# Kernel optimization log

Measured on AMD Instinct MI355X. Metric: run time of the kernel, lower is better.

The kernel has to match this reference:

```python
import jax, jax.numpy as jnp
import numpy as np
import math

NUM_SYN = 1000
NUM_MEM = 100
TAU_MIN, TAU_MAX = 10.0, 1000.0
TAU_S = 5.0
DELTA_T = 1.0
LAMBDA = 3.0

def _kappas():
    kappa_s = np.float32(np.exp(-DELTA_T / TAU_S))  # scalar (tau_s uniform)
    tau_m = np.logspace(math.log10(TAU_MIN + 1e-06), math.log10(TAU_MAX - 1e-06), NUM_MEM)
    kappa_m = np.exp(-DELTA_T / np.clip(tau_m, 1e-06, None)).astype(np.float32)
    return kappa_s, jnp.asarray(kappa_m)

def custom_tanh(x):
    return jnp.tanh(x * (2.0 / 3.0)) * 1.7159

def setup_inputs() -> dict:
    key = jax.random.key(0)
    ks = jax.random.split(key, 5)
    B, T = 128, 1024
    H = 2 * NUM_MEM  # 200
    X = jax.random.normal(ks[0], (B, T, NUM_SYN), dtype=jnp.float32)
    w_s = jnp.full((NUM_SYN,), 0.5, dtype=jnp.float32)
    W1 = jax.random.normal(ks[1], (NUM_SYN + NUM_MEM, H), dtype=jnp.float32) * 0.03
    b1 = jnp.zeros((H,), dtype=jnp.float32)
    W2 = jax.random.normal(ks[2], (H, NUM_MEM), dtype=jnp.float32) * 0.07
    b2 = jnp.zeros((NUM_MEM,), dtype=jnp.float32)
    Wy = jax.random.normal(ks[3], (NUM_MEM, 10), dtype=jnp.float32) * 0.1
    by = jnp.zeros((10,), dtype=jnp.float32)
    return {"X": X, "w_s": w_s, "W1": W1, "b1": b1, "W2": W2, "b2": b2, "Wy": Wy, "by": by}

def reference(X, w_s, W1, b1, W2, b2, Wy, by):
    kappa_s, kappa_m = _kappas()
    B = X.shape[0]
    w_s_pos = jax.nn.relu(w_s)

    def step(carry, x_t):
        s, m = carry  # s: [B, S], m: [B, M]
        s = kappa_s * s + w_s_pos * x_t
        km = kappa_m * m
        inp = jnp.concatenate([s, km], axis=-1)  # [B, S+M]
        h = jax.nn.relu(inp @ W1 + b1)
        dm = custom_tanh(h @ W2 + b2)
        m = km + LAMBDA * (1.0 - kappa_m) * dm
        y = m @ Wy + by
        return (s, m), y

    s0 = jnp.zeros((B, NUM_SYN), dtype=X.dtype)
    m0 = jnp.zeros((B, NUM_MEM), dtype=X.dtype)
    Xt = jnp.swapaxes(X, 0, 1)  # [T, B, S]
    _, ys = jax.lax.scan(step, (s0, m0), Xt)
    return jnp.swapaxes(ys, 0, 1)  # [B, T, num_output]
```

## Files before the change

kernel.cpp:

```cpp
#include <hip/hip_runtime.h>
#include <math.h>

#define SDIM 1000
#define KPAD 1024
#define HDIM 200
#define MDIM 100
#define NPAD 208
#define TSTEPS 1024
#define BATCH 128
#define MT (BATCH*TSTEPS)
#define TOTX ((size_t)MT*(size_t)SDIM)

#define Z_OFF 458752

typedef _Float16 half2_t __attribute__((ext_vector_type(2)));
typedef __attribute__((ext_vector_type(8))) short short8;
typedef __attribute__((ext_vector_type(4))) float f32x4;

static __device__ __forceinline__ unsigned short f2bf(float f) {
    unsigned u = __float_as_uint(f);
    unsigned r = 0x7fffu + ((u >> 16) & 1u);
    return (unsigned short)((u + r) >> 16);
}
static __device__ __forceinline__ float bf2f(unsigned short h) {
    return __uint_as_float((unsigned)h << 16);
}
static __device__ __forceinline__ half2_t as_h2(unsigned v) {
    union { unsigned u; half2_t h; } c; c.u = v; return c.h;
}
static __device__ __forceinline__ half2_t pk2(float a, float b) {
    half2_t r; r[0] = (_Float16)a; r[1] = (_Float16)b; return r;
}

static __device__ __forceinline__ void wg_barrier() {
    asm volatile("s_waitcnt lgkmcnt(0)" ::: "memory");
    __builtin_amdgcn_s_barrier();
    asm volatile("" ::: "memory");
}

__global__ __launch_bounds__(256) void prep_wpt(const float* __restrict__ w_s,
                                                const float* __restrict__ W1,
                                                unsigned short* __restrict__ wpt) {
    int idx = blockIdx.x * 256 + threadIdx.x;
    int n = idx >> 10, k = idx & (KPAD - 1);
    float v = 0.f;
    if (n < HDIM && k < SDIM) {
        float ws = fmaxf(w_s[k], 0.f);
        v = ws * W1[k * HDIM + n];
    }
    wpt[idx] = f2bf(v);
}

__global__ __launch_bounds__(256) void gemm_z(const float* __restrict__ X,
                                              const unsigned short* __restrict__ wpt,
                                              unsigned short* __restrict__ Z) {
    __shared__ __align__(16) unsigned short Abuf[2][128][40];
    __shared__ __align__(16) unsigned short Bbuf[2][13][16][40];
    const int t = threadIdx.x;
    const int m0 = blockIdx.x * 128;
    const int lane = t & 63, w = t >> 6;

    f32x4 acc[2][13];
#pragma unroll
    for (int mt = 0; mt < 2; ++mt)
#pragma unroll
        for (int i = 0; i < 13; ++i) acc[mt][i] = (f32x4){0.f, 0.f, 0.f, 0.f};

    auto stageA = [&](int bsel, int k0) {
        const int row = t >> 1, half = t & 1;
        size_t g = (size_t)(m0 + row) * SDIM + (size_t)(k0 + half * 16);
        float4 f0{}, f1{}, f2{}, f3{};
        if (g + 15 < TOTX) {
            f0 = *(const float4*)(X + g);      f1 = *(const float4*)(X + g + 4);
            f2 = *(const float4*)(X + g + 8);  f3 = *(const float4*)(X + g + 12);
        }
        short8 p0, p1;
        p0[0]=(short)f2bf(f0.x); p0[1]=(short)f2bf(f0.y); p0[2]=(short)f2bf(f0.z); p0[3]=(short)f2bf(f0.w);
        p0[4]=(short)f2bf(f1.x); p0[5]=(short)f2bf(f1.y); p0[6]=(short)f2bf(f1.z); p0[7]=(short)f2bf(f1.w);
        p1[0]=(short)f2bf(f2.x); p1[1]=(short)f2bf(f2.y); p1[2]=(short)f2bf(f2.z); p1[3]=(short)f2bf(f2.w);
        p1[4]=(short)f2bf(f3.x); p1[5]=(short)f2bf(f3.y); p1[6]=(short)f2bf(f3.z); p1[7]=(short)f2bf(f3.w);
        *(short8*)&Abuf[bsel][row][half * 16]     = p0;
        *(short8*)&Abuf[bsel][row][half * 16 + 8] = p1;
    };
    auto stageB = [&](int bsel, int k0) {
#pragma unroll
        for (int j = 0; j < 4; ++j) {
            int e = t + 256 * j;
            if (e < 832) {
                int n = e >> 2, q = e & 3;
                short8 v = *(const short8*)(wpt + (size_t)n * KPAD + k0 + q * 8);
                *(short8*)&Bbuf[bsel][n >> 4][n & 15][q * 8] = v;
            }
        }
    };

    stageA(0, 0);
    stageB(0, 0);
#pragma unroll 1
    for (int it = 0; it < 32; ++it) {
        __syncthreads();
        if (it + 1 < 32) { stageA((it + 1) & 1, (it + 1) * 32); stageB((it + 1) & 1, (it + 1) * 32); }
        const int bsel = it & 1;
        const short8 av0 = *(const short8*)&Abuf[bsel][w * 32 + (lane & 15)][(lane >> 4) * 8];
        const short8 av1 = *(const short8*)&Abuf[bsel][w * 32 + 16 + (lane & 15)][(lane >> 4) * 8];
#pragma unroll
        for (int nt = 0; nt < 13; ++nt) {
            const short8 bv = *(const short8*)&Bbuf[bsel][nt][lane & 15][(lane >> 4) * 8];
            acc[0][nt] = __builtin_amdgcn_mfma_f32_16x16x32_bf16(av0, bv, acc[0][nt], 0, 0, 0);
            acc[1][nt] = __builtin_amdgcn_mfma_f32_16x16x32_bf16(av1, bv, acc[1][nt], 0, 0, 0);
        }
    }

    const int colb = lane & 15;
#pragma unroll
    for (int mt = 0; mt < 2; ++mt) {
        const int rowb = m0 + w * 32 + mt * 16 + (lane >> 4) * 4;
#pragma unroll
        for (int nt = 0; nt < 13; ++nt) {
            int col = nt * 16 + colb;
            if (col < HDIM) {
#pragma unroll
                for (int r = 0; r < 4; ++r)
                    Z[(size_t)(rowb + r) * HDIM + col] = f2bf(acc[mt][nt][r]);
            }
        }
    }
}

__global__ __launch_bounds__(256, 1) void scan_seq(const unsigned short* __restrict__ Z,
        const float* __restrict__ W1, const float* __restrict__ b1,
        const float* __restrict__ W2, const float* __restrict__ b2,
        const float* __restrict__ Wy, const float* __restrict__ by,
        float* __restrict__ out) {
    __shared__ __align__(16) uint4 km4[2][13];
    __shared__ __align__(16) uint4 h4[25];
    __shared__ __align__(16) uint4 wyt4[10][13];

    const int t = threadIdx.x;
    const int b = blockIdx.x;

    if (t < 26) ((uint4*)km4)[t] = make_uint4(0, 0, 0, 0);

    float kapr = 0.f, cmr = 0.f, b2r = 0.f;
    if (t < MDIM) {
        double lg = 1.0000000434294482
                  + (double)t * ((2.9999999995657055 - 1.0000000434294482) / 99.0);
        double tau = exp(lg * 2.302585092994046);
        kapr = (float)exp(-1.0 / tau);
        cmr = 3.0f * (1.0f - kapr);
        b2r = b2[t];
        float inv = 1.0f / kapr;
#pragma unroll
        for (int o = 0; o < 10; ++o)
            ((_Float16*)wyt4[o])[t] = (_Float16)(Wy[t * 10 + o] * inv);
    } else if (t < 104) {
#pragma unroll
        for (int o = 0; o < 10; ++o) ((_Float16*)wyt4[o])[t] = (_Float16)0.f;
    }

    float b1r = (t < HDIM) ? b1[t] : 0.f;

    half2_t w1r[50];
#pragma unroll
    for (int c = 0; c < 50; ++c) {
        float a0 = 0.f, a1 = 0.f;
        if (t < HDIM) {
            a0 = W1[(SDIM + 2 * c) * HDIM + t];
            a1 = W1[(SDIM + 2 * c + 1) * HDIM + t];
        }
        w1r[c] = pk2(a0, a1);
    }

    half2_t w2r[100];
#pragma unroll
    for (int c = 0; c < 100; ++c) {
        float a0 = 0.f, a1 = 0.f;
        if (t < MDIM) {
            a0 = W2[(2 * c) * MDIM + t];
            a1 = W2[(2 * c + 1) * MDIM + t];
        }
        w2r[c] = pk2(a0, a1);
    }

    const int isY = (t >= 200 && t < 210);
    const int o = t - 200;
    float byr = isY ? by[o] : 0.f;

    const unsigned short* Zb = Z + (size_t)b * TSTEPS * HDIM;
    float* outb = out + (size_t)b * TSTEPS * 10;

    float u = 0.f;
    float m_kmn = 0.f;
    unsigned short zA = 0, zB = 0;
    if (t < HDIM) { zA = Zb[t]; zB = Zb[HDIM + t]; }

    __syncthreads();

    auto step = [&](const int CUR, const int PRV, unsigned short& zreg, const int st) {
        if (t < HDIM) {
            uint4 kp[13];
#pragma unroll
            for (int c = 0; c < 13; ++c) kp[c] = km4[PRV][c];
            u = 0.81873075307798182f * u + bf2f(zreg);
            int stn = st + 2; stn = (stn < TSTEPS) ? stn : TSTEPS - 1;
            zreg = Zb[(size_t)stn * HDIM + t];
            float a0 = u + b1r, a1 = 0.f, a2 = 0.f, a3 = 0.f;
#pragma unroll
            for (int c = 0; c < 13; ++c) {
                a0 = __builtin_amdgcn_fdot2(w1r[(4*c+0) % 50], as_h2(kp[c].x), a0, false);
                a1 = __builtin_amdgcn_fdot2(w1r[(4*c+1) % 50], as_h2(kp[c].y), a1, false);
                a2 = (4*c+2 < 50) ? __builtin_amdgcn_fdot2(w1r[4*c+2], as_h2(kp[c].z), a2, false) : a2;
                a3 = (4*c+3 < 50) ? __builtin_amdgcn_fdot2(w1r[4*c+3], as_h2(kp[c].w), a3, false) : a3;
            }
            float h = fmaxf((a0 + a1) + (a2 + a3), 0.f);
            ((_Float16*)h4)[t] = (_Float16)h;
        }
        wg_barrier();

        if (t < MDIM) {
            float e0 = 0.f, e1 = 0.f, e2 = 0.f, e3 = 0.f;
            uint4 hpA[13];
#pragma unroll
            for (int c = 0; c < 13; ++c) hpA[c] = h4[c];
#pragma unroll
            for (int c = 0; c < 13; ++c) {
                e0 = __builtin_amdgcn_fdot2(w2r[4*c+0], as_h2(hpA[c].x), e0, false);
                e1 = __builtin_amdgcn_fdot2(w2r[4*c+1], as_h2(hpA[c].y), e1, false);
                e2 = __builtin_amdgcn_fdot2(w2r[4*c+2], as_h2(hpA[c].z), e2, false);
                e3 = __builtin_amdgcn_fdot2(w2r[4*c+3], as_h2(hpA[c].w), e3, false);
            }
            uint4 hpB[12];
#pragma unroll
            for (int c = 0; c < 12; ++c) hpB[c] = h4[13 + c];
#pragma unroll
            for (int c = 0; c < 12; ++c) {
                e0 = __builtin_amdgcn_fdot2(w2r[52+4*c+0], as_h2(hpB[c].x), e0, false);
                e1 = __builtin_amdgcn_fdot2(w2r[52+4*c+1], as_h2(hpB[c].y), e1, false);
                e2 = __builtin_amdgcn_fdot2(w2r[52+4*c+2], as_h2(hpB[c].z), e2, false);
                e3 = __builtin_amdgcn_fdot2(w2r[52+4*c+3], as_h2(hpB[c].w), e3, false);
            }
            float s = (e0 + e1) + (e2 + e3);
            float x = (s + b2r) * (2.f / 3.f);
            float e = __expf(2.f * x);
            float dm = 1.7159f * (1.f - 2.f / (e + 1.f));
            float mnew = m_kmn + cmr * dm;
            m_kmn = kapr * mnew;
            ((_Float16*)km4[CUR])[t] = (_Float16)m_kmn;
        }

        if (isY && st > 0) {
            uint4 kmv[13], wyv[13];
#pragma unroll
            for (int c = 0; c < 13; ++c) { kmv[c] = km4[PRV][c]; wyv[c] = wyt4[o][c]; }
            float p0 = 0.f, p1 = 0.f, p2 = 0.f, p3 = 0.f;
#pragma unroll
            for (int c = 0; c < 13; ++c) {
                p0 = __builtin_amdgcn_fdot2(as_h2(wyv[c].x), as_h2(kmv[c].x), p0, false);
                p1 = __builtin_amdgcn_fdot2(as_h2(wyv[c].y), as_h2(kmv[c].y), p1, false);
                p2 = __builtin_amdgcn_fdot2(as_h2(wyv[c].z), as_h2(kmv[c].z), p2, false);
                p3 = __builtin_amdgcn_fdot2(as_h2(wyv[c].w), as_h2(kmv[c].w), p3, false);
            }
            outb[(size_t)(st - 1) * 10 + o] = (p0 + p1) + (p2 + p3) + byr;
        }
        wg_barrier();
    };

#pragma unroll 1
    for (int st = 0; st < TSTEPS; st += 2) {
        step(0, 1, zA, st);
        step(1, 0, zB, st + 1);
    }

    if (isY) {
        uint4 kmv[13], wyv[13];
#pragma unroll
        for (int c = 0; c < 13; ++c) { kmv[c] = km4[1][c]; wyv[c] = wyt4[o][c]; }
        float p0 = 0.f, p1 = 0.f, p2 = 0.f, p3 = 0.f;
#pragma unroll
        for (int c = 0; c < 13; ++c) {
            p0 = __builtin_amdgcn_fdot2(as_h2(wyv[c].x), as_h2(kmv[c].x), p0, false);
            p1 = __builtin_amdgcn_fdot2(as_h2(wyv[c].y), as_h2(kmv[c].y), p1, false);
            p2 = __builtin_amdgcn_fdot2(as_h2(wyv[c].z), as_h2(kmv[c].z), p2, false);
            p3 = __builtin_amdgcn_fdot2(as_h2(wyv[c].w), as_h2(kmv[c].w), p3, false);
        }
        outb[(size_t)(TSTEPS - 1) * 10 + o] = (p0 + p1) + (p2 + p3) + byr;
    }
}

extern "C" void kernel_launch(void* const* d_in, const int* in_sizes, int n_in,
                              void* d_out, int out_size, void* d_ws, size_t ws_size,
                              hipStream_t stream) {
    const float* X  = (const float*)d_in[0];
    const float* ws = (const float*)d_in[1];
    const float* W1 = (const float*)d_in[2];
    const float* b1 = (const float*)d_in[3];
    const float* W2 = (const float*)d_in[4];
    const float* b2 = (const float*)d_in[5];
    const float* Wy = (const float*)d_in[6];
    const float* by = (const float*)d_in[7];
    float* out = (float*)d_out;

    unsigned short* wpt = (unsigned short*)d_ws;
    unsigned short* Z   = (unsigned short*)((char*)d_ws + Z_OFF);

    hipLaunchKernelGGL(prep_wpt, dim3((NPAD * KPAD) / 256), dim3(256), 0, stream, ws, W1, wpt);
    hipLaunchKernelGGL(gemm_z, dim3(MT / 128), dim3(256), 0, stream, X, wpt, Z);
    hipLaunchKernelGGL(scan_seq, dim3(BATCH), dim3(256), 0, stream,
                       Z, W1, b1, W2, b2, Wy, by, out);
}
```

Before: 1.044 ms.

## Restructure scan step to use wave-local readlane broadcasts and one barrier per step

```diff
diff --git a/kernel.cpp b/kernel.cpp
--- a/kernel.cpp
+++ b/kernel.cpp
@@ -28,6 +28,9 @@
 static __device__ __forceinline__ half2_t as_h2(unsigned v) {
     union { unsigned u; half2_t h; } c; c.u = v; return c.h;
 }
+static __device__ __forceinline__ unsigned as_u32(half2_t h) {
+    union { half2_t h; unsigned u; } c; c.h = h; return c.u;
+}
 static __device__ __forceinline__ half2_t pk2(float a, float b) {
     half2_t r; r[0] = (_Float16)a; r[1] = (_Float16)b; return r;
 }
@@ -132,158 +135,144 @@
         const float* __restrict__ W2, const float* __restrict__ b2,
         const float* __restrict__ Wy, const float* __restrict__ by,
         float* __restrict__ out) {
-    __shared__ __align__(16) uint4 km4[2][13];
-    __shared__ __align__(16) uint4 h4[25];
-    __shared__ __align__(16) uint4 wyt4[10][13];
+    __shared__ __align__(16) float part[2][4][104];
+    __shared__ float kap_s[104], cm_s[104];
 
     const int t = threadIdx.x;
     const int b = blockIdx.x;
-
-    if (t < 26) ((uint4*)km4)[t] = make_uint4(0, 0, 0, 0);
-
-    float kapr = 0.f, cmr = 0.f, b2r = 0.f;
-    if (t < MDIM) {
-        double lg = 1.0000000434294482
-                  + (double)t * ((2.9999999995657055 - 1.0000000434294482) / 99.0);
-        double tau = exp(lg * 2.302585092994046);
-        kapr = (float)exp(-1.0 / tau);
-        cmr = 3.0f * (1.0f - kapr);
-        b2r = b2[t];
-        float inv = 1.0f / kapr;
-#pragma unroll
-        for (int o = 0; o < 10; ++o)
-            ((_Float16*)wyt4[o])[t] = (_Float16)(Wy[t * 10 + o] * inv);
-    } else if (t < 104) {
-#pragma unroll
-        for (int o = 0; o < 10; ++o) ((_Float16*)wyt4[o])[t] = (_Float16)0.f;
-    }
-
-    float b1r = (t < HDIM) ? b1[t] : 0.f;
+    const int w = t >> 6, lane = t & 63;
+    const int n = 50 * w + lane;
+    const bool hAct = lane < 50;
+    const bool yAct = (w == 0) && (lane >= 50 && lane < 60);
+    const int o = lane - 50;
+
+    if (t < 104) {
+        float kv = 0.f, cv = 0.f;
+        if (t < MDIM) {
+            double lg = 1.0000000434294482
+                      + (double)t * ((2.9999999995657055 - 1.0000000434294482) / 99.0);
+            double tau = exp(lg * 2.302585092994046);
+            kv = (float)exp(-1.0 / tau);
+            cv = 3.0f * (1.0f - kv);
+        }
+        kap_s[t] = kv; cm_s[t] = cv;
+    }
+    __syncthreads();
 
     half2_t w1r[50];
 #pragma unroll
     for (int c = 0; c < 50; ++c) {
         float a0 = 0.f, a1 = 0.f;
-        if (t < HDIM) {
-            a0 = W1[(SDIM + 2 * c) * HDIM + t];
-            a1 = W1[(SDIM + 2 * c + 1) * HDIM + t];
+        if (hAct) {
+            a0 = kap_s[2 * c]     * W1[(SDIM + 2 * c)     * HDIM + n];
+            a1 = kap_s[2 * c + 1] * W1[(SDIM + 2 * c + 1) * HDIM + n];
+        } else if (yAct) {
+            a0 = Wy[(2 * c) * 10 + o];
+            a1 = Wy[(2 * c + 1) * 10 + o];
         }
         w1r[c] = pk2(a0, a1);
     }
-
-    half2_t w2r[100];
-#pragma unroll
-    for (int c = 0; c < 100; ++c) {
-        float a0 = 0.f, a1 = 0.f;
-        if (t < MDIM) {
-            a0 = W2[(2 * c) * MDIM + t];
-            a1 = W2[(2 * c + 1) * MDIM + t];
-        }
-        w2r[c] = pk2(a0, a1);
-    }
-
-    const int isY = (t >= 200 && t < 210);
-    const int o = t - 200;
-    float byr = isY ? by[o] : 0.f;
+    float base_b = hAct ? b1[n] : (yAct ? by[o] : 0.f);
+
+    const int j0 = 2 * lane, j1 = 2 * lane + 1;
+    half2_t w2r[50];
+#pragma unroll
+    for (int c = 0; c < 25; ++c) {
+        float a00 = 0.f, a10 = 0.f, a01 = 0.f, a11 = 0.f;
+        if (hAct) {
+            int k0 = 50 * w + 2 * c, k1 = k0 + 1;
+            a00 = W2[k0 * MDIM + j0]; a10 = W2[k1 * MDIM + j0];
+            a01 = W2[k0 * MDIM + j1]; a11 = W2[k1 * MDIM + j1];
+        }
+        w2r[2 * c]     = pk2(a00, a10);
+        w2r[2 * c + 1] = pk2(a01, a11);
+    }
+
+    float kap0 = 0.f, kap1 = 0.f, cm0 = 0.f, cm1 = 0.f, b20 = 0.f, b21 = 0.f;
+    if (hAct) {
+        kap0 = kap_s[j0]; kap1 = kap_s[j1];
+        cm0 = cm_s[j0];   cm1 = cm_s[j1];
+        b20 = b2[j0];     b21 = b2[j1];
+    }
 
     const unsigned short* Zb = Z + (size_t)b * TSTEPS * HDIM;
     float* outb = out + (size_t)b * TSTEPS * 10;
 
-    float u = 0.f;
-    float m_kmn = 0.f;
+    float u = 0.f, m0 = 0.f, m1 = 0.f;
     unsigned short zA = 0, zB = 0;
-    if (t < HDIM) { zA = Zb[t]; zB = Zb[HDIM + t]; }
+    if (hAct) { zA = Zb[n]; zB = Zb[HDIM + n]; }
+
+    int sm[50];
+#pragma unroll
+    for (int c = 0; c < 50; ++c) sm[c] = 0;
 
     __syncthreads();
 
-    auto step = [&](const int CUR, const int PRV, unsigned short& zreg, const int st) {
-        if (t < HDIM) {
-            uint4 kp[13];
-#pragma unroll
-            for (int c = 0; c < 13; ++c) kp[c] = km4[PRV][c];
+    auto stepf = [&](const int P, unsigned short& zreg, const int st) {
+        float acc = base_b;
+        if (hAct) {
             u = 0.81873075307798182f * u + bf2f(zreg);
             int stn = st + 2; stn = (stn < TSTEPS) ? stn : TSTEPS - 1;
-            zreg = Zb[(size_t)stn * HDIM + t];
-            float a0 = u + b1r, a1 = 0.f, a2 = 0.f, a3 = 0.f;
-#pragma unroll
-            for (int c = 0; c < 13; ++c) {
-                a0 = __builtin_amdgcn_fdot2(w1r[(4*c+0) % 50], as_h2(kp[c].x), a0, false);
-                a1 = __builtin_amdgcn_fdot2(w1r[(4*c+1) % 50], as_h2(kp[c].y), a1, false);
-                a2 = (4*c+2 < 50) ? __builtin_amdgcn_fdot2(w1r[4*c+2], as_h2(kp[c].z), a2, false) : a2;
-                a3 = (4*c+3 < 50) ? __builtin_amdgcn_fdot2(w1r[4*c+3], as_h2(kp[c].w), a3, false) : a3;
+            zreg = Zb[(size_t)stn * HDIM + n];
+            acc += u;
+        }
+        float r = acc;
+        if (hAct || yAct) {
+#pragma unroll
+            for (int c = 0; c < 50; ++c)
+                r = __builtin_amdgcn_fdot2(w1r[c], as_h2((unsigned)sm[c]), r, false);
+        }
+        if (yAct && st > 0) outb[(size_t)(st - 1) * 10 + o] = r;
+        float h = fmaxf(r, 0.f);
+
+        float ho = __shfl_xor(h, 1);
+        unsigned hpk = as_u32(pk2(h, ho));
+        int sh[25];
+#pragma unroll
+        for (int c = 0; c < 25; ++c) sh[c] = __builtin_amdgcn_readlane((int)hpk, 2 * c);
+
+        if (hAct) {
+            float a0 = 0.f, a1 = 0.f;
+#pragma unroll
+            for (int c = 0; c < 25; ++c) {
+                a0 = __builtin_amdgcn_fdot2(w2r[2 * c],     as_h2((unsigned)sh[c]), a0, false);
+                a1 = __builtin_amdgcn_fdot2(w2r[2 * c + 1], as_h2((unsigned)sh[c]), a1, false);
             }
-            float h = fmaxf((a0 + a1) + (a2 + a3), 0.f);
-            ((_Float16*)h4)[t] = (_Float16)h;
+            *(float2*)&part[P][w][j0] = make_float2(a0, a1);
         }
         wg_barrier();
 
-        if (t < MDIM) {
-            float e0 = 0.f, e1 = 0.f, e2 = 0.f, e3 = 0.f;
-            uint4 hpA[13];
-#pragma unroll
-            for (int c = 0; c < 13; ++c) hpA[c] = h4[c];
-#pragma unroll
-            for (int c = 0; c < 13; ++c) {
-                e0 = __builtin_amdgcn_fdot2(w2r[4*c+0], as_h2(hpA[c].x), e0, false);
-                e1 = __builtin_amdgcn_fdot2(w2r[4*c+1], as_h2(hpA[c].y), e1, false);
-                e2 = __builtin_amdgcn_fdot2(w2r[4*c+2], as_h2(hpA[c].z), e2, false);
-                e3 = __builtin_amdgcn_fdot2(w2r[4*c+3], as_h2(hpA[c].w), e3, false);
-            }
-            uint4 hpB[12];
-#pragma unroll
-            for (int c = 0; c < 12; ++c) hpB[c] = h4[13 + c];
-#pragma unroll
-            for (int c = 0; c < 12; ++c) {
-                e0 = __builtin_amdgcn_fdot2(w2r[52+4*c+0], as_h2(hpB[c].x), e0, false);
-                e1 = __builtin_amdgcn_fdot2(w2r[52+4*c+1], as_h2(hpB[c].y), e1, false);
-                e2 = __builtin_amdgcn_fdot2(w2r[52+4*c+2], as_h2(hpB[c].z), e2, false);
-                e3 = __builtin_amdgcn_fdot2(w2r[52+4*c+3], as_h2(hpB[c].w), e3, false);
-            }
-            float s = (e0 + e1) + (e2 + e3);
-            float x = (s + b2r) * (2.f / 3.f);
-            float e = __expf(2.f * x);
-            float dm = 1.7159f * (1.f - 2.f / (e + 1.f));
-            float mnew = m_kmn + cmr * dm;
-            m_kmn = kapr * mnew;
-            ((_Float16*)km4[CUR])[t] = (_Float16)m_kmn;
-        }
-
-        if (isY && st > 0) {
-            uint4 kmv[13], wyv[13];
-#pragma unroll
-            for (int c = 0; c < 13; ++c) { kmv[c] = km4[PRV][c]; wyv[c] = wyt4[o][c]; }
-            float p0 = 0.f, p1 = 0.f, p2 = 0.f, p3 = 0.f;
-#pragma unroll
-            for (int c = 0; c < 13; ++c) {
-                p0 = __builtin_amdgcn_fdot2(as_h2(wyv[c].x), as_h2(kmv[c].x), p0, false);
-                p1 = __builtin_amdgcn_fdot2(as_h2(wyv[c].y), as_h2(kmv[c].y), p1, false);
-                p2 = __builtin_amdgcn_fdot2(as_h2(wyv[c].z), as_h2(kmv[c].z), p2, false);
-                p3 = __builtin_amdgcn_fdot2(as_h2(wyv[c].w), as_h2(kmv[c].w), p3, false);
-            }
-            outb[(size_t)(st - 1) * 10 + o] = (p0 + p1) + (p2 + p3) + byr;
-        }
-        wg_barrier();
+        if (hAct) {
+            float2 q0 = *(const float2*)&part[P][0][j0];
+            float2 q1 = *(const float2*)&part[P][1][j0];
+            float2 q2 = *(const float2*)&part[P][2][j0];
+            float2 q3 = *(const float2*)&part[P][3][j0];
+            float s0 = ((q0.x + q1.x) + (q2.x + q3.x)) + b20;
+            float s1 = ((q0.y + q1.y) + (q2.y + q3.y)) + b21;
+            float x0 = s0 * (2.f / 3.f), x1 = s1 * (2.f / 3.f);
+            float e0 = __expf(2.f * x0), e1 = __expf(2.f * x1);
+            float dm0 = 1.7159f * (1.f - 2.f / (e0 + 1.f));
+            float dm1 = 1.7159f * (1.f - 2.f / (e1 + 1.f));
+            m0 = kap0 * m0 + cm0 * dm0;
+            m1 = kap1 * m1 + cm1 * dm1;
+        }
+        unsigned mpk = as_u32(pk2(m0, m1));
+#pragma unroll
+        for (int c = 0; c < 50; ++c) sm[c] = __builtin_amdgcn_readlane((int)mpk, c);
     };
 
 #pragma unroll 1
     for (int st = 0; st < TSTEPS; st += 2) {
-        step(0, 1, zA, st);
-        step(1, 0, zB, st + 1);
-    }
-
-    if (isY) {
-        uint4 kmv[13], wyv[13];
-#pragma unroll
-        for (int c = 0; c < 13; ++c) { kmv[c] = km4[1][c]; wyv[c] = wyt4[o][c]; }
-        float p0 = 0.f, p1 = 0.f, p2 = 0.f, p3 = 0.f;
-#pragma unroll
-        for (int c = 0; c < 13; ++c) {
-            p0 = __builtin_amdgcn_fdot2(as_h2(wyv[c].x), as_h2(kmv[c].x), p0, false);
-            p1 = __builtin_amdgcn_fdot2(as_h2(wyv[c].y), as_h2(kmv[c].y), p1, false);
-            p2 = __builtin_amdgcn_fdot2(as_h2(wyv[c].z), as_h2(kmv[c].z), p2, false);
-            p3 = __builtin_amdgcn_fdot2(as_h2(wyv[c].w), as_h2(kmv[c].w), p3, false);
-        }
-        outb[(size_t)(TSTEPS - 1) * 10 + o] = (p0 + p1) + (p2 + p3) + byr;
+        stepf(0, zA, st);
+        stepf(1, zB, st + 1);
+    }
+
+    if (yAct) {
+        float r = base_b;
+#pragma unroll
+        for (int c = 0; c < 50; ++c)
+            r = __builtin_amdgcn_fdot2(w1r[c], as_h2((unsigned)sm[c]), r, false);
+        outb[(size_t)(TSTEPS - 1) * 10 + o] = r;
     }
 }
 
```

Measured after the change: 1.038 ms, median of 3. About the same (-0.6%).
